# Kernel optimization log

Hardware: AMD Instinct MI355X
Metric: run time of the kernel (lower is better)

The kernel has to match this reference:

```python
import jax, jax.numpy as jnp
import numpy as np

D_MODEL = 1024
NUM_HEADS = 16
MAX_SEQ_LEN = 2048
BATCH = 4
SEQ_LEN = 2048


def setup_inputs() -> dict:
    key = jax.random.key(0)
    ks = jax.random.split(key, 7)
    s = 0.02
    return {
        "x": jax.random.normal(ks[0], (BATCH, SEQ_LEN, D_MODEL), dtype=jnp.float32),
        "Wq": jax.random.normal(ks[1], (D_MODEL, D_MODEL), dtype=jnp.float32) * s,
        "Wk": jax.random.normal(ks[2], (D_MODEL, D_MODEL), dtype=jnp.float32) * s,
        "Wv": jax.random.normal(ks[3], (D_MODEL, D_MODEL), dtype=jnp.float32) * s,
        "Wo": jax.random.normal(ks[4], (D_MODEL, D_MODEL), dtype=jnp.float32) * s,
        "bo": jnp.zeros((D_MODEL,), dtype=jnp.float32),
        "bias_table": jax.random.normal(ks[5], (2 * MAX_SEQ_LEN - 1, NUM_HEADS), dtype=jnp.float32) * s,
    }


def reference(x, Wq, Wk, Wv, Wo, bo, bias_table):
    B, S, D = x.shape
    H = NUM_HEADS
    hd = D // H
    scale = hd ** -0.5

    # torch Linear: y = x @ W.T
    q = (x @ Wq.T).reshape(B, S, H, hd).transpose(0, 2, 1, 3)  # [B,H,S,hd]
    k = (x @ Wk.T).reshape(B, S, H, hd).transpose(0, 2, 1, 3)
    v = (x @ Wv.T).reshape(B, S, H, hd).transpose(0, 2, 1, 3)

    scores = jnp.einsum("bhqd,bhkd->bhqk", q, k) * scale  # [B,H,S,S]

    # relative index: coords[:,None] - coords[None,:] + max_seq_len - 1
    coords = jnp.arange(S)
    rel_idx = coords[:, None] - coords[None, :] + MAX_SEQ_LEN - 1  # [S,S]
    rel_bias = bias_table[rel_idx]              # [S,S,H]
    rel_bias = rel_bias.transpose(2, 0, 1)[None]  # [1,H,S,S]

    probs = jax.nn.softmax(scores + rel_bias, axis=-1)
    ctx = jnp.einsum("bhqk,bhkd->bhqd", probs, v)  # [B,H,S,hd]
    ctx = ctx.transpose(0, 2, 1, 3).reshape(B, S, D)
    return ctx @ Wo.T + bo
```

## Files before the change

kernel.cpp:

```cpp
#include <hip/hip_runtime.h>
#include <string.h>

typedef unsigned short u16;
typedef unsigned int   u32;
typedef __attribute__((ext_vector_type(8))) short short8;
typedef __attribute__((ext_vector_type(4))) float f32x4;
typedef __attribute__((ext_vector_type(2))) __fp16 h2;
typedef __attribute__((ext_vector_type(4))) __fp16 h4;

__device__ __forceinline__ u16 f2b(float f) {
  u32 u = __float_as_uint(f);
  u32 r = (u + 0x7fffu + ((u >> 16) & 1u)) >> 16;
  return (u16)r;
}
__device__ __forceinline__ void cp16(const u16* g, u16* l) {
  __builtin_amdgcn_global_load_lds(
      (const __attribute__((address_space(1))) void*)g,
      (__attribute__((address_space(3))) void*)l, 16, 0, 0);
}

__global__ __launch_bounds__(256) void cvt_f2b_kernel(const float* __restrict__ in,
                                                      u16* __restrict__ out, int n) {
  int i = (blockIdx.x * 256 + threadIdx.x) * 4;
  if (i + 3 < n) {
    float4 v = *(const float4*)&in[i];
    ushort4 o = make_ushort4(f2b(v.x), f2b(v.y), f2b(v.z), f2b(v.w));
    *(ushort4*)&out[i] = o;
  }
}
__global__ __launch_bounds__(256) void cvtw_kernel(const float* __restrict__ w0,
                                                   const float* __restrict__ w1,
                                                   const float* __restrict__ w2,
                                                   const float* __restrict__ w3,
                                                   u16* __restrict__ out) {
  const float* src = (blockIdx.y == 0) ? w0 : (blockIdx.y == 1) ? w1
                   : (blockIdx.y == 2) ? w2 : w3;
  int i = (blockIdx.x * 256 + threadIdx.x) * 4;
  float4 v = *(const float4*)&src[i];
  ushort4 o = make_ushort4(f2b(v.x), f2b(v.y), f2b(v.z), f2b(v.w));
  *(ushort4*)&out[(size_t)blockIdx.y * 1048576 + i] = o;
}

template<int MODE>
__global__ __launch_bounds__(256) void gemm128_bt(
    const u16* __restrict__ A, const u16* __restrict__ Bw,
    void* __restrict__ outp, const float* __restrict__ bias,
    const int M, const int N, const int K) {
  __shared__ __attribute__((aligned(16))) u16 As[2][128 * 32];
  __shared__ __attribute__((aligned(16))) u16 Bs[2][128 * 32];

  const u16* Bw2 = Bw;
  if (MODE == 0) Bw2 += ((size_t)blockIdx.z) << 20;

  const int tid  = threadIdx.x;
  const int wave = tid >> 6, lane = tid & 63;
  const int quad = lane >> 4, l15 = lane & 15;
  const int wm   = (wave >> 1) * 64, wn = (wave & 1) * 64;
  const int m0   = blockIdx.x * 128, n0 = blockIdx.y * 128;

  const int srow = wave * 32 + (lane >> 2);
  const int scol = (lane & 3) * 8;
  const u16* gA0 = A   + (size_t)(m0 + srow) * K + scol;
  const u16* gA1 = gA0 + (size_t)16 * K;
  const u16* gB0 = Bw2 + (size_t)(n0 + srow) * K + scol;
  const u16* gB1 = gB0 + (size_t)16 * K;
  const int lo0 = (wave * 32) * 32, lo1 = (wave * 32 + 16) * 32;

  cp16(gA0, &As[0][lo0]); cp16(gA1, &As[0][lo1]);
  cp16(gB0, &Bs[0][lo0]); cp16(gB1, &Bs[0][lo1]);
  gA0 += 32; gA1 += 32; gB0 += 32; gB1 += 32;

  f32x4 acc[4][4] = {};
  const int nk = K >> 5;
  for (int kt = 0; kt < nk; ++kt) {
    const int cur = kt & 1;
    __syncthreads();
    if (kt + 1 < nk) {
      cp16(gA0, &As[1 - cur][lo0]); cp16(gA1, &As[1 - cur][lo1]);
      cp16(gB0, &Bs[1 - cur][lo0]); cp16(gB1, &Bs[1 - cur][lo1]);
      gA0 += 32; gA1 += 32; gB0 += 32; gB1 += 32;
    }
    short8 af[4], bf[4];
    #pragma unroll
    for (int mi = 0; mi < 4; ++mi)
      af[mi] = *(const short8*)&As[cur][(wm + mi * 16 + l15) * 32 + quad * 8];
    #pragma unroll
    for (int ni = 0; ni < 4; ++ni)
      bf[ni] = *(const short8*)&Bs[cur][(wn + ni * 16 + l15) * 32 + quad * 8];
    #pragma unroll
    for (int mi = 0; mi < 4; ++mi)
      #pragma unroll
      for (int ni = 0; ni < 4; ++ni)
        acc[mi][ni] = __builtin_amdgcn_mfma_f32_16x16x32_bf16(af[mi], bf[ni], acc[mi][ni], 0, 0, 0);
  }

  #pragma unroll
  for (int mi = 0; mi < 4; ++mi)
    #pragma unroll
    for (int ni = 0; ni < 4; ++ni) {
      if (MODE == 0 && blockIdx.z == 2) {
        int mb = m0 + wm + mi * 16 + quad * 4;
        int n  = n0 + wn + ni * 16 + l15;
        int b = mb >> 11, s = mb & 2047, h = n >> 6, d = n & 63;
        u16* out = (u16*)outp + (((size_t)2) << 23);
        h2 p0 = __builtin_amdgcn_cvt_pkrtz(acc[mi][ni][0], acc[mi][ni][1]);
        h2 p1 = __builtin_amdgcn_cvt_pkrtz(acc[mi][ni][2], acc[mi][ni][3]);
        ushort4 o;
        memcpy(&o.x, &p0, 4);
        memcpy(&o.z, &p1, 4);
        *(ushort4*)&out[((((size_t)b * 16 + h) * 64 + d) << 11) + s] = o;
      } else {
        #pragma unroll
        for (int r = 0; r < 4; ++r) {
          int m = m0 + wm + mi * 16 + quad * 4 + r;
          int n = n0 + wn + ni * 16 + l15;
          float v = acc[mi][ni][r];
          if (MODE == 0) {
            int b = m >> 11, s = m & 2047, h = n >> 6, d = n & 63;
            u16* out = (u16*)outp + (((size_t)blockIdx.z) << 23);
            out[((((size_t)b * 16 + h) * 2048 + s) << 6) + d] = f2b(v);
          } else {
            ((float*)outp)[(size_t)m * N + n] = v + bias[n];
          }
        }
      }
    }
}

__global__ __launch_bounds__(256, 4) void attn_mfma_kernel(
    const u16* __restrict__ qb, const u16* __restrict__ kb, const u16* __restrict__ vtb,
    const float* __restrict__ bias_table, u16* __restrict__ ctx) {
  __shared__ __attribute__((aligned(16))) u16 Ks[2][64 * 64];
  __shared__ __attribute__((aligned(16))) u16 Vs[64][72];
  __shared__ __attribute__((aligned(16))) float bias_s[2304];

  const int tid  = threadIdx.x;
  const int wave = tid >> 6, lane = tid & 63;
  const int quad = lane >> 4, l15 = lane & 15;
  const int bh   = blockIdx.x, h = bh & 15, b = bh >> 4;
  const int q0   = blockIdx.y * 128;

  for (int i = tid; i < 2175; i += 256)
    bias_s[i] = bias_table[(q0 + i) * 16 + h] * 1.44269504f;

  short8 aQ[2][2];
  #pragma unroll
  for (int qt = 0; qt < 2; ++qt)
    #pragma unroll
    for (int ks = 0; ks < 2; ++ks)
      aQ[qt][ks] = *(const short8*)&qb[((size_t)bh * 2048 + q0 + wave * 32 + qt * 16 + l15) * 64
                                       + ks * 32 + quad * 8];

  const h4 onesh = {(__fp16)1.f, (__fp16)1.f, (__fp16)1.f, (__fp16)1.f};

  f32x4 accO[4][2] = {};
  f32x4 accL[2]    = {};

  const int krow = lane >> 3;
  const int kchk = (lane & 7) ^ krow;
  const u16* kbase = kb + (((size_t)bh * 2048) << 6);
  const int xsw = l15 & 7;

  const int srow = tid >> 2, t0 = tid & 3;
  const u16* vrow = vtb + (((size_t)bh * 64 + srow) << 11) + t0 * 16;

  short8 vpre0 = *(const short8*)&vrow[0];
  short8 vpre1 = *(const short8*)&vrow[8];
  #pragma unroll
  for (int g = 0; g < 2; ++g)
    cp16(kbase + (size_t)(wave * 16 + g * 8 + krow) * 64 + kchk * 8,
         &Ks[0][(wave * 16 + g * 8) * 64]);

  for (int kt = 0; kt < 32; ++kt) {
    const int cur = kt & 1;
    __syncthreads();
    {
      ushort4 w0, w1, w2, w3;
      memcpy(&w0, &vpre0, 8);  memcpy(&w1, ((const char*)&vpre0) + 8, 8);
      memcpy(&w2, &vpre1, 8);  memcpy(&w3, ((const char*)&vpre1) + 8, 8);
      *(ushort4*)&Vs[srow][ 0 + t0 * 4] = w0;
      *(ushort4*)&Vs[srow][16 + t0 * 4] = w1;
      *(ushort4*)&Vs[srow][32 + t0 * 4] = w2;
      *(ushort4*)&Vs[srow][48 + t0 * 4] = w3;
    }
    __syncthreads();
    if (kt < 31) {
      const u16* vp = vrow + ((kt + 1) << 6);
      vpre0 = *(const short8*)&vp[0];
      vpre1 = *(const short8*)&vp[8];
      #pragma unroll
      for (int g = 0; g < 2; ++g)
        cp16(kbase + (size_t)((kt + 1) * 64 + wave * 16 + g * 8 + krow) * 64 + kchk * 8,
             &Ks[1 - cur][(wave * 16 + g * 8) * 64]);
    }

    const int k0 = kt * 64;

    short8 bK[4][2];
    #pragma unroll
    for (int nt = 0; nt < 4; ++nt)
      #pragma unroll
      for (int ks = 0; ks < 2; ++ks)
        bK[nt][ks] = *(const short8*)&Ks[cur][(nt * 16 + l15) * 64
                                             + (((ks * 4 + quad) ^ xsw) << 3)];
    f32x4 accS[4][2] = {};
    #pragma unroll
    for (int nt = 0; nt < 4; ++nt)
      #pragma unroll
      for (int qt = 0; qt < 2; ++qt) {
        accS[nt][qt] = __builtin_amdgcn_mfma_f32_16x16x32_bf16(bK[nt][0], aQ[qt][0], accS[nt][qt], 0, 0, 0);
        accS[nt][qt] = __builtin_amdgcn_mfma_f32_16x16x32_bf16(bK[nt][1], aQ[qt][1], accS[nt][qt], 0, 0, 0);
      }

    h4 bP[2][4];
    #pragma unroll
    for (int qt = 0; qt < 2; ++qt)
      #pragma unroll
      for (int nt = 0; nt < 4; ++nt) {
        const int jbm = (wave * 32 + qt * 16 + l15) - (nt * 16 + quad * 4) - k0 + 2044;
        float bb0 = bias_s[jbm],     bb1 = bias_s[jbm + 1];
        float bb2 = bias_s[jbm + 2], bb3 = bias_s[jbm + 3];
        float p0 = __builtin_amdgcn_exp2f(fmaf(accS[nt][qt][0], 0.18033688f, bb3));
        float p1 = __builtin_amdgcn_exp2f(fmaf(accS[nt][qt][1], 0.18033688f, bb2));
        float p2 = __builtin_amdgcn_exp2f(fmaf(accS[nt][qt][2], 0.18033688f, bb1));
        float p3 = __builtin_amdgcn_exp2f(fmaf(accS[nt][qt][3], 0.18033688f, bb0));
        h2 e01 = __builtin_amdgcn_cvt_pkrtz(p0, p1);
        h2 e23 = __builtin_amdgcn_cvt_pkrtz(p2, p3);
        h4 bp;
        bp[0] = e01[0]; bp[1] = e01[1]; bp[2] = e23[0]; bp[3] = e23[1];
        bP[qt][nt] = bp;
        accL[qt] = __builtin_amdgcn_mfma_f32_16x16x16f16(onesh, bp, accL[qt], 0, 0, 0);
      }

    #pragma unroll
    for (int dt = 0; dt < 4; ++dt) {
      short8 v0 = *(const short8*)&Vs[dt * 16 + l15][quad * 16];
      short8 v1 = *(const short8*)&Vs[dt * 16 + l15][quad * 16 + 8];
      h4 aV[4];
      memcpy(&aV[0], &v0, 8);  memcpy(&aV[1], ((const char*)&v0) + 8, 8);
      memcpy(&aV[2], &v1, 8);  memcpy(&aV[3], ((const char*)&v1) + 8, 8);
      #pragma unroll
      for (int qt = 0; qt < 2; ++qt)
        #pragma unroll
        for (int nt = 0; nt < 4; ++nt)
          accO[dt][qt] = __builtin_amdgcn_mfma_f32_16x16x16f16(aV[nt], bP[qt][nt], accO[dt][qt], 0, 0, 0);
    }
  }

  #pragma unroll
  for (int qt = 0; qt < 2; ++qt) {
    const float inv = 1.0f / accL[qt][0];
    const int q = q0 + wave * 32 + qt * 16 + l15;
    #pragma unroll
    for (int dt = 0; dt < 4; ++dt) {
      ushort4 o = make_ushort4(f2b(accO[dt][qt][0] * inv), f2b(accO[dt][qt][1] * inv),
                               f2b(accO[dt][qt][2] * inv), f2b(accO[dt][qt][3] * inv));
      *(ushort4*)&ctx[((size_t)b * 2048 + q) * 1024 + h * 64 + dt * 16 + quad * 4] = o;
    }
  }
}

extern "C" void kernel_launch(void* const* d_in, const int* in_sizes, int n_in,
                              void* d_out, int out_size, void* d_ws, size_t ws_size,
                              hipStream_t stream) {
  const float* x          = (const float*)d_in[0];
  const float* Wq         = (const float*)d_in[1];
  const float* Wk         = (const float*)d_in[2];
  const float* Wv         = (const float*)d_in[3];
  const float* Wo         = (const float*)d_in[4];
  const float* bo         = (const float*)d_in[5];
  const float* bias_table = (const float*)d_in[6];
  float* out = (float*)d_out;

  char* ws = (char*)d_ws;
  u16* xb   = (u16*)(ws);
  u16* wqb  = (u16*)(ws + 16777216);
  u16* wob  = (u16*)(ws + 16777216 + 3 * 2097152);
  u16* qb   = (u16*)(ws + 25165824);
  u16* kb   = qb + 8388608;
  u16* vtb  = kb + 8388608;
  u16* ctxb = (u16*)(ws + 75497472);

  cvt_f2b_kernel<<<8192, 256, 0, stream>>>(x, xb, 8388608);
  cvtw_kernel<<<dim3(1024, 4), 256, 0, stream>>>(Wq, Wk, Wv, Wo, wqb);

  gemm128_bt<0><<<dim3(64, 8, 3), 256, 0, stream>>>(
      xb, wqb, (void*)qb, nullptr, 8192, 1024, 1024);

  attn_mfma_kernel<<<dim3(64, 16), 256, 0, stream>>>(qb, kb, vtb, bias_table, ctxb);

  gemm128_bt<1><<<dim3(64, 8), 256, 0, stream>>>(
      ctxb, wob, (void*)out, bo, 8192, 1024, 1024);
}
```

Before: 291.5 us.

## Switch attention kernel to 32x32 MFMA tiles with permlane-swapped P fragments

```diff
diff --git a/kernel.cpp b/kernel.cpp
--- a/kernel.cpp
+++ b/kernel.cpp
@@ -5,8 +5,10 @@
 typedef unsigned int   u32;
 typedef __attribute__((ext_vector_type(8))) short short8;
 typedef __attribute__((ext_vector_type(4))) float f32x4;
+typedef __attribute__((ext_vector_type(16))) float f32x16;
 typedef __attribute__((ext_vector_type(2))) __fp16 h2;
-typedef __attribute__((ext_vector_type(4))) __fp16 h4;
+typedef __attribute__((ext_vector_type(8))) __fp16 h8;
+typedef __attribute__((ext_vector_type(2))) unsigned int u32x2;
 
 __device__ __forceinline__ u16 f2b(float f) {
   u32 u = __float_as_uint(f);
@@ -17,6 +19,10 @@
   __builtin_amdgcn_global_load_lds(
       (const __attribute__((address_space(1))) void*)g,
       (__attribute__((address_space(3))) void*)l, 16, 0, 0);
+}
+__device__ __forceinline__ void plswap(u32& a, u32& b) {
+  u32x2 r = __builtin_amdgcn_permlane32_swap(a, b, false, false);
+  a = r[0]; b = r[1];
 }
 
 __global__ __launch_bounds__(256) void cvt_f2b_kernel(const float* __restrict__ in,
@@ -131,38 +137,36 @@
     const u16* __restrict__ qb, const u16* __restrict__ kb, const u16* __restrict__ vtb,
     const float* __restrict__ bias_table, u16* __restrict__ ctx) {
   __shared__ __attribute__((aligned(16))) u16 Ks[2][64 * 64];
-  __shared__ __attribute__((aligned(16))) u16 Vs[64][72];
+  __shared__ __attribute__((aligned(16))) u16 Vs[64 * 64];
   __shared__ __attribute__((aligned(16))) float bias_s[2304];
 
   const int tid  = threadIdx.x;
   const int wave = tid >> 6, lane = tid & 63;
-  const int quad = lane >> 4, l15 = lane & 15;
+  const int l31  = lane & 31, hi = lane >> 5;
+  const int xsw  = l31 & 7;
   const int bh   = blockIdx.x, h = bh & 15, b = bh >> 4;
   const int q0   = blockIdx.y * 128;
 
   for (int i = tid; i < 2175; i += 256)
     bias_s[i] = bias_table[(q0 + i) * 16 + h] * 1.44269504f;
 
-  short8 aQ[2][2];
-  #pragma unroll
-  for (int qt = 0; qt < 2; ++qt)
-    #pragma unroll
-    for (int ks = 0; ks < 2; ++ks)
-      aQ[qt][ks] = *(const short8*)&qb[((size_t)bh * 2048 + q0 + wave * 32 + qt * 16 + l15) * 64
-                                       + ks * 32 + quad * 8];
-
-  const h4 onesh = {(__fp16)1.f, (__fp16)1.f, (__fp16)1.f, (__fp16)1.f};
-
-  f32x4 accO[4][2] = {};
-  f32x4 accL[2]    = {};
+  short8 aQ[4];
+  #pragma unroll
+  for (int ks = 0; ks < 4; ++ks)
+    aQ[ks] = *(const short8*)&qb[((size_t)bh * 2048 + q0 + wave * 32 + l31) * 64
+                                 + ks * 16 + hi * 8];
+
+  f32x16 accO[2] = {};
+  float  lsum = 0.f;
 
   const int krow = lane >> 3;
   const int kchk = (lane & 7) ^ krow;
   const u16* kbase = kb + (((size_t)bh * 2048) << 6);
-  const int xsw = l15 & 7;
-
-  const int srow = tid >> 2, t0 = tid & 3;
+
+  const int srow = tid >> 2, t0 = tid & 3, ssw = srow & 7;
   const u16* vrow = vtb + (((size_t)bh * 64 + srow) << 11) + t0 * 16;
+  const int vo0 = srow * 64 + (((2 * t0    ) ^ ssw) << 3);
+  const int vo1 = srow * 64 + (((2 * t0 + 1) ^ ssw) << 3);
 
   short8 vpre0 = *(const short8*)&vrow[0];
   short8 vpre1 = *(const short8*)&vrow[8];
@@ -174,18 +178,11 @@
   for (int kt = 0; kt < 32; ++kt) {
     const int cur = kt & 1;
     __syncthreads();
-    {
-      ushort4 w0, w1, w2, w3;
-      memcpy(&w0, &vpre0, 8);  memcpy(&w1, ((const char*)&vpre0) + 8, 8);
-      memcpy(&w2, &vpre1, 8);  memcpy(&w3, ((const char*)&vpre1) + 8, 8);
-      *(ushort4*)&Vs[srow][ 0 + t0 * 4] = w0;
-      *(ushort4*)&Vs[srow][16 + t0 * 4] = w1;
-      *(ushort4*)&Vs[srow][32 + t0 * 4] = w2;
-      *(ushort4*)&Vs[srow][48 + t0 * 4] = w3;
-    }
+    *(short8*)&Vs[vo0] = vpre0;
+    *(short8*)&Vs[vo1] = vpre1;
     __syncthreads();
     if (kt < 31) {
-      const u16* vp = vrow + ((kt + 1) << 6);
+      const u16* vp = vrow + ((size_t)(kt + 1) << 6);
       vpre0 = *(const short8*)&vp[0];
       vpre1 = *(const short8*)&vp[8];
       #pragma unroll
@@ -194,70 +191,61 @@
              &Ks[1 - cur][(wave * 16 + g * 8) * 64]);
     }
 
-    const int k0 = kt * 64;
-
-    short8 bK[4][2];
-    #pragma unroll
-    for (int nt = 0; nt < 4; ++nt)
-      #pragma unroll
-      for (int ks = 0; ks < 2; ++ks)
-        bK[nt][ks] = *(const short8*)&Ks[cur][(nt * 16 + l15) * 64
-                                             + (((ks * 4 + quad) ^ xsw) << 3)];
-    f32x4 accS[4][2] = {};
-    #pragma unroll
-    for (int nt = 0; nt < 4; ++nt)
-      #pragma unroll
-      for (int qt = 0; qt < 2; ++qt) {
-        accS[nt][qt] = __builtin_amdgcn_mfma_f32_16x16x32_bf16(bK[nt][0], aQ[qt][0], accS[nt][qt], 0, 0, 0);
-        accS[nt][qt] = __builtin_amdgcn_mfma_f32_16x16x32_bf16(bK[nt][1], aQ[qt][1], accS[nt][qt], 0, 0, 0);
-      }
-
-    h4 bP[2][4];
-    #pragma unroll
-    for (int qt = 0; qt < 2; ++qt)
-      #pragma unroll
-      for (int nt = 0; nt < 4; ++nt) {
-        const int jbm = (wave * 32 + qt * 16 + l15) - (nt * 16 + quad * 4) - k0 + 2044;
-        float bb0 = bias_s[jbm],     bb1 = bias_s[jbm + 1];
-        float bb2 = bias_s[jbm + 2], bb3 = bias_s[jbm + 3];
-        float p0 = __builtin_amdgcn_exp2f(fmaf(accS[nt][qt][0], 0.18033688f, bb3));
-        float p1 = __builtin_amdgcn_exp2f(fmaf(accS[nt][qt][1], 0.18033688f, bb2));
-        float p2 = __builtin_amdgcn_exp2f(fmaf(accS[nt][qt][2], 0.18033688f, bb1));
-        float p3 = __builtin_amdgcn_exp2f(fmaf(accS[nt][qt][3], 0.18033688f, bb0));
-        h2 e01 = __builtin_amdgcn_cvt_pkrtz(p0, p1);
-        h2 e23 = __builtin_amdgcn_cvt_pkrtz(p2, p3);
-        h4 bp;
-        bp[0] = e01[0]; bp[1] = e01[1]; bp[2] = e23[0]; bp[3] = e23[1];
-        bP[qt][nt] = bp;
-        accL[qt] = __builtin_amdgcn_mfma_f32_16x16x16f16(onesh, bp, accL[qt], 0, 0, 0);
-      }
-
-    #pragma unroll
-    for (int dt = 0; dt < 4; ++dt) {
-      short8 v0 = *(const short8*)&Vs[dt * 16 + l15][quad * 16];
-      short8 v1 = *(const short8*)&Vs[dt * 16 + l15][quad * 16 + 8];
-      h4 aV[4];
-      memcpy(&aV[0], &v0, 8);  memcpy(&aV[1], ((const char*)&v0) + 8, 8);
-      memcpy(&aV[2], &v1, 8);  memcpy(&aV[3], ((const char*)&v1) + 8, 8);
-      #pragma unroll
-      for (int qt = 0; qt < 2; ++qt)
+    #pragma unroll
+    for (int t = 0; t < 2; ++t) {
+      f32x16 accS = {};
+      #pragma unroll
+      for (int ks = 0; ks < 4; ++ks) {
+        short8 aK = *(const short8*)&Ks[cur][(t * 32 + l31) * 64
+                                            + (((ks * 2 + hi) ^ xsw) << 3)];
+        accS = __builtin_amdgcn_mfma_f32_32x32x16_bf16(aK, aQ[ks], accS, 0, 0, 0);
+      }
+
+      u32 d[8];
+      const int ib = wave * 32 + l31 - kt * 64 - t * 32 - 4 * hi + 2047;
+      #pragma unroll
+      for (int rg = 0; rg < 4; ++rg) {
+        const int bb = ib - 8 * rg;
+        float p0 = __builtin_amdgcn_exp2f(fmaf(accS[4 * rg + 0], 0.18033688f, bias_s[bb    ]));
+        float p1 = __builtin_amdgcn_exp2f(fmaf(accS[4 * rg + 1], 0.18033688f, bias_s[bb - 1]));
+        float p2 = __builtin_amdgcn_exp2f(fmaf(accS[4 * rg + 2], 0.18033688f, bias_s[bb - 2]));
+        float p3 = __builtin_amdgcn_exp2f(fmaf(accS[4 * rg + 3], 0.18033688f, bias_s[bb - 3]));
+        lsum += (p0 + p1) + (p2 + p3);
+        h2 e0; e0[0] = (__fp16)p0; e0[1] = (__fp16)p1;
+        h2 e1; e1[0] = (__fp16)p2; e1[1] = (__fp16)p3;
+        memcpy(&d[2 * rg],     &e0, 4);
+        memcpy(&d[2 * rg + 1], &e1, 4);
+      }
+
+      #pragma unroll
+      for (int sl = 0; sl < 2; ++sl) {
+        u32 F0 = d[4 * sl], F1 = d[4 * sl + 1], F2 = d[4 * sl + 2], F3 = d[4 * sl + 3];
+        plswap(F0, F2);
+        plswap(F1, F3);
+        union { u32 w[4]; h8 v; } uf;
+        uf.w[0] = F0; uf.w[1] = F1; uf.w[2] = F2; uf.w[3] = F3;
+        const int ch = ((t * 2 + sl) * 2 + hi) ^ xsw;
         #pragma unroll
-        for (int nt = 0; nt < 4; ++nt)
-          accO[dt][qt] = __builtin_amdgcn_mfma_f32_16x16x16f16(aV[nt], bP[qt][nt], accO[dt][qt], 0, 0, 0);
+        for (int dt = 0; dt < 2; ++dt) {
+          short8 av = *(const short8*)&Vs[(dt * 32 + l31) * 64 + (ch << 3)];
+          h8 avh; memcpy(&avh, &av, 16);
+          accO[dt] = __builtin_amdgcn_mfma_f32_32x32x16_f16(avh, uf.v, accO[dt], 0, 0, 0);
+        }
+      }
     }
   }
 
-  #pragma unroll
-  for (int qt = 0; qt < 2; ++qt) {
-    const float inv = 1.0f / accL[qt][0];
-    const int q = q0 + wave * 32 + qt * 16 + l15;
-    #pragma unroll
-    for (int dt = 0; dt < 4; ++dt) {
-      ushort4 o = make_ushort4(f2b(accO[dt][qt][0] * inv), f2b(accO[dt][qt][1] * inv),
-                               f2b(accO[dt][qt][2] * inv), f2b(accO[dt][qt][3] * inv));
-      *(ushort4*)&ctx[((size_t)b * 2048 + q) * 1024 + h * 64 + dt * 16 + quad * 4] = o;
-    }
-  }
+  const float ltot = lsum + __shfl_xor(lsum, 32);
+  const float inv  = 1.0f / ltot;
+  const int q = q0 + wave * 32 + l31;
+  #pragma unroll
+  for (int dt = 0; dt < 2; ++dt)
+    #pragma unroll
+    for (int rg = 0; rg < 4; ++rg) {
+      ushort4 o = make_ushort4(f2b(accO[dt][4 * rg + 0] * inv), f2b(accO[dt][4 * rg + 1] * inv),
+                               f2b(accO[dt][4 * rg + 2] * inv), f2b(accO[dt][4 * rg + 3] * inv));
+      *(ushort4*)&ctx[((size_t)b * 2048 + q) * 1024 + h * 64 + dt * 32 + rg * 8 + hi * 4] = o;
+    }
 }
 
 extern "C" void kernel_launch(void* const* d_in, const int* in_sizes, int n_in,
```

Result: no change. 293.4 us (+0.6%).
